# Kernel optimization log

Hardware: AMD Instinct MI355X
Metric: run time of the kernel (lower is better)

The kernel has to match this reference:

```python
import jax, jax.numpy as jnp
import numpy as np

B = 32
STRIDES = (8, 16, 32, 64, 128)
FEATS = ((192, 192), (96, 96), (48, 48), (24, 24), (12, 12))
IMG_H = IMG_W = 1536.0
OCTAVE_SCALE = 8.0
SCORE_THR = 0.05
IOU_THR = 0.6
MAX_NUM = 100
NMS_PRE = 1000
C = 2  # num foreground classes
RCLIP = float(np.log(1000.0 / 16.0))  # wh_ratio_clip from delta2bbox


def setup_inputs() -> dict:
    key = jax.random.key(0)
    ks = jax.random.split(key, 15)
    inp = {}
    i = 0
    for l, (h, w) in enumerate(FEATS):
        inp[f"cls{l}"] = jax.random.normal(ks[i], (B, C, h, w), jnp.float32); i += 1
        inp[f"bbox{l}"] = jax.random.normal(ks[i], (B, 4, h, w), jnp.float32) * 0.5; i += 1
        inp[f"ctr{l}"] = jax.random.normal(ks[i], (B, 1, h, w), jnp.float32); i += 1
    return inp


def _anchors(h, w, stride):
    # one square anchor of side OCTAVE_SCALE*stride per grid location
    xs = jnp.arange(w, dtype=jnp.float32) * stride
    ys = jnp.arange(h, dtype=jnp.float32) * stride
    cx = jnp.broadcast_to(xs[None, :], (h, w))
    cy = jnp.broadcast_to(ys[:, None], (h, w))
    half = 0.5 * OCTAVE_SCALE * stride
    return jnp.stack([cx - half, cy - half, cx + half, cy + half], -1).reshape(-1, 4)


def _decode(anchors, deltas):
    # standard delta2bbox (means=0, stds=1), clipped to image
    aw = anchors[..., 2] - anchors[..., 0]
    ah = anchors[..., 3] - anchors[..., 1]
    acx = anchors[..., 0] + 0.5 * aw
    acy = anchors[..., 1] + 0.5 * ah
    dx, dy = deltas[..., 0], deltas[..., 1]
    dw = jnp.clip(deltas[..., 2], -RCLIP, RCLIP)
    dh = jnp.clip(deltas[..., 3], -RCLIP, RCLIP)
    pcx = acx + dx * aw
    pcy = acy + dy * ah
    pw = aw * jnp.exp(dw)
    ph = ah * jnp.exp(dh)
    x1 = jnp.clip(pcx - 0.5 * pw, 0.0, IMG_W)
    y1 = jnp.clip(pcy - 0.5 * ph, 0.0, IMG_H)
    x2 = jnp.clip(pcx + 0.5 * pw, 0.0, IMG_W)
    y2 = jnp.clip(pcy + 0.5 * ph, 0.0, IMG_H)
    return jnp.stack([x1, y1, x2, y2], -1)


def _nms_single(boxes, boxes_off, scores, labels):
    # greedy class-aware NMS with fixed MAX_NUM output slots
    areas = (boxes_off[:, 2] - boxes_off[:, 0]) * (boxes_off[:, 3] - boxes_off[:, 1])

    def step(s, _):
        i = jnp.argmax(s)
        sc = s[i]
        valid = sc > 0.0
        b = boxes_off[i]
        ix1 = jnp.maximum(b[0], boxes_off[:, 0])
        iy1 = jnp.maximum(b[1], boxes_off[:, 1])
        ix2 = jnp.minimum(b[2], boxes_off[:, 2])
        iy2 = jnp.minimum(b[3], boxes_off[:, 3])
        inter = jnp.maximum(ix2 - ix1, 0.0) * jnp.maximum(iy2 - iy1, 0.0)
        iou = inter / jnp.maximum(areas[i] + areas - inter, 1e-6)
        s_new = jnp.where(valid & (iou > IOU_THR), -1.0, s)
        det = jnp.where(valid, jnp.concatenate([boxes[i], sc[None]]), jnp.zeros(5, jnp.float32))
        lab = jnp.where(valid, labels[i], -1)
        return s_new, (det, lab)

    _, (dets, labs) = jax.lax.scan(step, scores, None, length=MAX_NUM)
    return dets, labs


def _forward(cls0, cls1, cls2, cls3, cls4, bbox0, bbox1, bbox2, bbox3, bbox4,
             ctr0, ctr1, ctr2, ctr3, ctr4):
    clss = (cls0, cls1, cls2, cls3, cls4)
    bbs = (bbox0, bbox1, bbox2, bbox3, bbox4)
    ctrs = (ctr0, ctr1, ctr2, ctr3, ctr4)
    boxes_l, scores_l, ctr_l = [], [], []
    for (h, w), stride, cl, bb, ct in zip(FEATS, STRIDES, clss, bbs, ctrs):
        hw = h * w
        s = jax.nn.sigmoid(cl.reshape(B, C, hw).transpose(0, 2, 1))  # [B,HW,C]
        c = jax.nn.sigmoid(ct.reshape(B, hw))                        # [B,HW]
        d = bb.reshape(B, 4, hw).transpose(0, 2, 1)                  # [B,HW,4]
        anch = _anchors(h, w, stride)                                # [HW,4]
        k = min(NMS_PRE, hw)
        _, idx = jax.lax.top_k(s.max(-1) * c, k)                     # [B,k] nms_pre pre-selection
        s = jnp.take_along_axis(s, idx[..., None], 1)
        d = jnp.take_along_axis(d, idx[..., None], 1)
        c = jnp.take_along_axis(c, idx, 1)
        boxes_l.append(_decode(anch[idx], d))
        scores_l.append(s)
        ctr_l.append(c)
    boxes = jnp.concatenate(boxes_l, 1)    # [B,M,4]
    scores = jnp.concatenate(scores_l, 1)  # [B,M,C]
    ctr = jnp.concatenate(ctr_l, 1)        # [B,M]

    # multiclass_nms: scores * centerness factor, threshold, class-offset NMS
    cand_scores = (scores * ctr[..., None]).reshape(B, -1)              # [B,M*C]
    cand_scores = jnp.where(cand_scores > SCORE_THR, cand_scores, -1.0)
    cand_boxes = jnp.repeat(boxes, C, axis=1)                           # [B,M*C,4]
    labels = jnp.tile(jnp.arange(C, dtype=jnp.int32), boxes.shape[1])   # [M*C]
    offset = labels.astype(jnp.float32) * (IMG_W + 1.0)
    cand_off = cand_boxes + offset[None, :, None]
    dets, labs = jax.vmap(lambda b, bo, s: _nms_single(b, bo, s, labels))(
        cand_boxes, cand_off, cand_scores)
    return dets, labs  # [B,MAX_NUM,5] fp32, [B,MAX_NUM] int32 (-1 = empty slot)


def reference(cls0, cls1, cls2, cls3, cls4, bbox0, bbox1, bbox2, bbox3, bbox4,
              ctr0, ctr1, ctr2, ctr3, ctr4):
    return _forward(cls0, cls1, cls2, cls3, cls4, bbox0, bbox1, bbox2, bbox3, bbox4,
                    ctr0, ctr1, ctr2, ctr3, ctr4)
```

## Files before the change

### kernel.cpp

```cpp
#include <hip/hip_runtime.h>
#include <stdint.h>

#define BATCH 32
#define M_TOT 3720
#define NCAND 7440
#define NPAD 8192
#define SCORE_THR 0.05f
#define IOU_THR 0.6f
#define RCLIP 4.135166556742356f
#define IMG 1536.0f

__device__ __forceinline__ float sigf(float x) {
    return __fdiv_rn(1.0f, __fadd_rn(1.0f, expf(-x)));
}

struct P5 { const float* p[5]; };

template <int NPT>
__device__ __forceinline__ void select_level(
    const float* __restrict__ cls, const float* __restrict__ ctr,
    int b, int hw, int take, unsigned short* __restrict__ slots_out,
    unsigned long long* cu, unsigned* hist, unsigned* wtot,
    unsigned& sh_bin, unsigned& sh_krem, unsigned& sh_cnt)
{
    const int tid = threadIdx.x;
    float kv[NPT];
#pragma unroll
    for (int r = 0; r < NPT; ++r) {
        int i = tid + r * 1024;
        if (i < hw) {
            float s0 = sigf(cls[(size_t)(2*b)*hw + i]);
            float s1 = sigf(cls[(size_t)(2*b+1)*hw + i]);
            float sc = sigf(ctr[(size_t)b*hw + i]);
            kv[r] = __fmul_rn(fmaxf(s0, s1), sc);
        } else {
            kv[r] = -1.0f;
        }
    }

    int n;
    if (hw > 1000) {
        unsigned pref = 0, krem = 1000;
        for (int p = 0; p < 4; ++p) {
            const int shift = 24 - 8 * p;
            if (tid < 256) hist[tid] = 0;
            __syncthreads();
#pragma unroll
            for (int r = 0; r < NPT; ++r) {
                int i = tid + r * 1024;
                if (i < hw) {
                    unsigned u = __float_as_uint(kv[r]);
                    bool match = (p == 0) || ((u >> (shift + 8)) == pref);
                    if (match) atomicAdd(&hist[(u >> shift) & 255u], 1u);
                }
            }
            __syncthreads();
            unsigned h = 0, s = 0;
            if (tid < 256) {
                h = hist[tid];
                s = h;
#pragma unroll
                for (int d = 1; d < 64; d <<= 1) {
                    unsigned o = __shfl_down(s, d);
                    if ((tid & 63) + d < 64) s += o;
                }
                if ((tid & 63) == 0) wtot[tid >> 6] = s;
            }
            __syncthreads();
            if (tid < 256) {
                unsigned hi = 0;
                int wv = tid >> 6;
                for (int w2 = wv + 1; w2 < 4; ++w2) hi += wtot[w2];
                unsigned suf_incl = s + hi;
                unsigned suf_excl = suf_incl - h;
                if (suf_excl < krem && suf_incl >= krem) {
                    sh_bin = (unsigned)tid;
                    sh_krem = krem - suf_excl;
                    sh_cnt = 0;
                }
            }
            __syncthreads();
            pref = (pref << 8) | sh_bin;
            krem = sh_krem;
        }
        const unsigned T = pref;
#pragma unroll
        for (int r = 0; r < NPT; ++r) {
            int i = tid + r * 1024;
            if (i < hw) {
                unsigned u = __float_as_uint(kv[r]);
                if (u >= T) {
                    unsigned pos = atomicAdd(&sh_cnt, 1u);
                    if (pos < 2048u)
                        cu[pos] = (((unsigned long long)u) << 20) | (unsigned)(0xFFFFF - i);
                }
            }
        }
        __syncthreads();
        n = (int)sh_cnt; if (n > 2048) n = 2048;
    } else {
#pragma unroll
        for (int r = 0; r < NPT; ++r) {
            int i = tid + r * 1024;
            if (i < hw) {
                unsigned u = __float_as_uint(kv[r]);
                cu[i] = (((unsigned long long)u) << 20) | (unsigned)(0xFFFFF - i);
            }
        }
        n = hw;
        __syncthreads();
    }
    for (int a = tid; a < n; a += 1024) {
        unsigned long long ka = cu[a];
        int rank = 0;
        for (int q = 0; q < n; ++q) rank += (cu[q] > ka) ? 1 : 0;
        if (rank < take) {
            unsigned loc = 0xFFFFFu - (unsigned)(ka & 0xFFFFFu);
            slots_out[rank] = (unsigned short)loc;
        }
    }
}

__global__ __launch_bounds__(1024) void k_select(P5 CLS, P5 CT,
                                                 unsigned short* __restrict__ slots_g) {
    __shared__ unsigned long long cu[2048];
    __shared__ unsigned hist[256];
    __shared__ unsigned wtot[4];
    __shared__ unsigned sh_bin, sh_krem, sh_cnt;

    const int HWs[5]  = {36864, 9216, 2304, 576, 144};
    const int MOFF[5] = {0, 1000, 2000, 3000, 3576};

    const int blk = blockIdx.x;
    const int b = blk / 5, l = blk % 5;
    const int hw = HWs[l];
    const int take = (hw < 1000) ? hw : 1000;
    unsigned short* slots_out = slots_g + (size_t)b * M_TOT + MOFF[l];

    if (l == 0)      select_level<36>(CLS.p[0], CT.p[0], b, hw, take, slots_out, cu, hist, wtot, sh_bin, sh_krem, sh_cnt);
    else if (l == 1) select_level<9> (CLS.p[1], CT.p[1], b, hw, take, slots_out, cu, hist, wtot, sh_bin, sh_krem, sh_cnt);
    else if (l == 2) select_level<3> (CLS.p[2], CT.p[2], b, hw, take, slots_out, cu, hist, wtot, sh_bin, sh_krem, sh_cnt);
    else if (l == 3) select_level<1> (CLS.p[3], CT.p[3], b, hw, take, slots_out, cu, hist, wtot, sh_bin, sh_krem, sh_cnt);
    else             select_level<1> (CLS.p[4], CT.p[4], b, hw, take, slots_out, cu, hist, wtot, sh_bin, sh_krem, sh_cnt);
}

__global__ __launch_bounds__(256) void k_decode(P5 CLS, P5 BB, P5 CT,
                                                const unsigned short* __restrict__ slots_g,
                                                float* __restrict__ boxes_g,
                                                float* __restrict__ scores_g) {
    const int HWs[5]  = {36864, 9216, 2304, 576, 144};
    const int Ws[5]   = {192, 96, 48, 24, 12};
    const int STRs[5] = {8, 16, 32, 64, 128};
    int t = blockIdx.x * blockDim.x + threadIdx.x;
    if (t >= BATCH * M_TOT) return;
    int b = t / M_TOT;
    int m = t - b * M_TOT;
    int l;
    if (m < 1000)      l = 0;
    else if (m < 2000) l = 1;
    else if (m < 3000) l = 2;
    else if (m < 3576) l = 3;
    else               l = 4;
    const int hw = HWs[l], w = Ws[l], stride = STRs[l];
    int loc = slots_g[t];

    float ctv = sigf(CT.p[l][(size_t)b*hw + loc]);
    float sc0 = __fmul_rn(sigf(CLS.p[l][(size_t)(2*b+0)*hw + loc]), ctv);
    float sc1 = __fmul_rn(sigf(CLS.p[l][(size_t)(2*b+1)*hw + loc]), ctv);
    scores_g[(size_t)b * NCAND + 2*m + 0] = (sc0 > SCORE_THR) ? sc0 : -1.0f;
    scores_g[(size_t)b * NCAND + 2*m + 1] = (sc1 > SCORE_THR) ? sc1 : -1.0f;

    int yy = loc / w;
    int xx = loc - yy * w;
    const float* bb = BB.p[l];
    float d0 = bb[(size_t)(4*b+0)*hw + loc];
    float d1 = bb[(size_t)(4*b+1)*hw + loc];
    float d2 = bb[(size_t)(4*b+2)*hw + loc];
    float d3 = bb[(size_t)(4*b+3)*hw + loc];
    float a   = (float)(8 * stride);
    float acx = (float)(xx * stride);
    float acy = (float)(yy * stride);
    float dwv = fminf(fmaxf(d2, -RCLIP), RCLIP);
    float dhv = fminf(fmaxf(d3, -RCLIP), RCLIP);
    float pcx = __fadd_rn(acx, __fmul_rn(d0, a));
    float pcy = __fadd_rn(acy, __fmul_rn(d1, a));
    float pw  = __fmul_rn(a, expf(dwv));
    float ph  = __fmul_rn(a, expf(dhv));
    float* bx = boxes_g + (size_t)t * 4;
    bx[0] = fminf(fmaxf(__fsub_rn(pcx, __fmul_rn(0.5f, pw)), 0.0f), IMG);
    bx[1] = fminf(fmaxf(__fsub_rn(pcy, __fmul_rn(0.5f, ph)), 0.0f), IMG);
    bx[2] = fminf(fmaxf(__fadd_rn(pcx, __fmul_rn(0.5f, pw)), 0.0f), IMG);
    bx[3] = fminf(fmaxf(__fadd_rn(pcy, __fmul_rn(0.5f, ph)), 0.0f), IMG);
}

__global__ __launch_bounds__(1024) void k_nms(const float* __restrict__ boxes_g,
                                              const float* __restrict__ scores_g,
                                              float* __restrict__ out) {
    __shared__ unsigned long long cu[NPAD];
    const int b = blockIdx.x, tid = threadIdx.x;

    unsigned long long v[8];
    if (tid < 930) {
        const float4* s4 = (const float4*)(scores_g + (size_t)b * NCAND) + tid * 2;
        float4 a4 = s4[0], c4 = s4[1];
        float ss[8] = {a4.x, a4.y, a4.z, a4.w, c4.x, c4.y, c4.z, c4.w};
#pragma unroll
        for (int r = 0; r < 8; ++r) {
            int i = tid * 8 + r;
            v[r] = (ss[r] > 0.0f)
                ? ((((unsigned long long)(~__float_as_uint(ss[r]))) << 16) | (unsigned)i)
                : ~0ULL;
        }
    } else {
#pragma unroll
        for (int r = 0; r < 8; ++r) v[r] = ~0ULL;
    }

    for (unsigned kk = 2; kk <= NPAD; kk <<= 1) {
        for (unsigned j = kk >> 1; j > 0; j >>= 1) {
            if (j >= 512) {
                __syncthreads();
#pragma unroll
                for (int r = 0; r < 8; ++r) cu[tid * 8 + r] = v[r];
                __syncthreads();
#pragma unroll
                for (int r = 0; r < 8; ++r) {
                    unsigned i = tid * 8 + r;
                    unsigned long long pv = cu[i ^ j];
                    bool up = ((i & kk) == 0);
                    bool lower = ((i & j) == 0);
                    bool keepmin = (lower == up);
                    v[r] = keepmin ? (v[r] < pv ? v[r] : pv)
                                   : (v[r] > pv ? v[r] : pv);
                }
            } else if (j >= 8) {
                unsigned m = j >> 3;
#pragma unroll
                for (int r = 0; r < 8; ++r) {
                    unsigned long long pv = __shfl_xor(v[r], (int)m, 64);
                    unsigned i = tid * 8 + r;
                    bool up = ((i & kk) == 0);
                    bool lower = ((i & j) == 0);
                    bool keepmin = (lower == up);
                    v[r] = keepmin ? (v[r] < pv ? v[r] : pv)
                                   : (v[r] > pv ? v[r] : pv);
                }
            } else {
#pragma unroll
                for (int r = 0; r < 8; ++r) {
                    if ((r & j) == 0) {
                        unsigned i = tid * 8 + r;
                        bool up = ((i & kk) == 0);
                        unsigned long long a = v[r], b2 = v[r | j];
                        if ((a > b2) == up) { v[r] = b2; v[r | j] = a; }
                    }
                }
            }
        }
    }
    __syncthreads();
#pragma unroll
    for (int r = 0; r < 8; ++r) cu[tid * 8 + r] = v[r];
    __syncthreads();

    if (tid >= 64) return;

    const int lane = tid;
    const float4* bx4 = (const float4*)(boxes_g + (size_t)b * M_TOT * 4);
    float* keptL = (float*)(cu + NCAND);

    int kc = 0;
    bool done = false;

    for (int base = 0; base < NCAND && kc < 100 && !done; base += 64) {
        unsigned long long e = (base + lane < NCAND) ? cu[base + lane] : ~0ULL;
        bool valid = (e != ~0ULL);
        unsigned myidx = (unsigned)(e & 0xFFFFull);
        float myscore = __uint_as_float(~(unsigned)(e >> 16));
        int myc = (int)(myidx & 1u);
        float bx1 = 0, by1 = 0, bx2 = 0, by2 = 0;
        if (valid) {
            float4 vv = bx4[myidx >> 1];
            bx1 = vv.x; by1 = vv.y; bx2 = vv.z; by2 = vv.w;
        }
        float offv = myc ? (IMG + 1.0f) : 0.0f;
        float ox1 = __fadd_rn(bx1, offv), oy1 = __fadd_rn(by1, offv);
        float ox2 = __fadd_rn(bx2, offv), oy2 = __fadd_rn(by2, offv);
        float ca = __fmul_rn(__fsub_rn(ox2, ox1), __fsub_rn(oy2, oy1));
        float uni_s = fmaxf(__fsub_rn(__fadd_rn(ca, ca), ca), 1e-6f);
        bool mySticky = !(__fdiv_rn(ca, uni_s) > IOU_THR);

        const bool hasInvalid = (__ballot(!valid) != 0ULL);

        bool ov = false;
        if (valid) {
            for (int k = 0; k < kc && !ov; ++k) {
                float px1 = keptL[k*5+0], py1 = keptL[k*5+1];
                float px2 = keptL[k*5+2], py2 = keptL[k*5+3];
                float pa  = keptL[k*5+4];
                float ix1 = fmaxf(px1, ox1), iy1 = fmaxf(py1, oy1);
                float ix2 = fminf(px2, ox2), iy2 = fminf(py2, oy2);
                float inter = __fmul_rn(fmaxf(__fsub_rn(ix2, ix1), 0.0f),
                                        fmaxf(__fsub_rn(iy2, iy1), 0.0f));
                float uni = fmaxf(__fsub_rn(__fadd_rn(pa, ca), inter), 1e-6f);
                ov = (__fdiv_rn(inter, uni) > IOU_THR);
            }
        }
        bool myAlive = valid && !ov;
        unsigned long long aliveMask = __ballot(myAlive);

        while (aliveMask != 0ULL && kc < 100) {
            int j = __ffsll(aliveMask) - 1;
            float pbx1 = __shfl(bx1, j), pby1 = __shfl(by1, j);
            float pbx2 = __shfl(bx2, j), pby2 = __shfl(by2, j);
            float pox1 = __shfl(ox1, j), poy1 = __shfl(oy1, j);
            float pox2 = __shfl(ox2, j), poy2 = __shfl(oy2, j);
            float pca  = __shfl(ca, j);
            float psc  = __shfl(myscore, j);
            int   pc   = __shfl(myc, j);
            int   pst  = __shfl((int)mySticky, j);

            if (pst) {
                for (int t2 = kc + lane; t2 < 100; t2 += 64) {
                    float* dr = out + ((size_t)b * 100 + t2) * 5;
                    dr[0] = pbx1; dr[1] = pby1; dr[2] = pbx2; dr[3] = pby2; dr[4] = psc;
                    out[(size_t)BATCH * 500 + b * 100 + t2] = (float)pc;
                }
                kc = 100;
                done = true;
                break;
            }
            if (lane == 0) {
                float* dr = out + ((size_t)b * 100 + kc) * 5;
                dr[0] = pbx1; dr[1] = pby1; dr[2] = pbx2; dr[3] = pby2; dr[4] = psc;
                out[(size_t)BATCH * 500 + b * 100 + kc] = (float)pc;
                keptL[kc*5+0] = pox1; keptL[kc*5+1] = poy1;
                keptL[kc*5+2] = pox2; keptL[kc*5+3] = poy2;
                keptL[kc*5+4] = pca;
            }
            ++kc;
            if (myAlive && lane > j) {
                float ix1 = fmaxf(pox1, ox1), iy1 = fmaxf(poy1, oy1);
                float ix2 = fminf(pox2, ox2), iy2 = fminf(poy2, oy2);
                float inter = __fmul_rn(fmaxf(__fsub_rn(ix2, ix1), 0.0f),
                                        fmaxf(__fsub_rn(iy2, iy1), 0.0f));
                float uni = fmaxf(__fsub_rn(__fadd_rn(pca, ca), inter), 1e-6f);
                if (__fdiv_rn(inter, uni) > IOU_THR) myAlive = false;
            }
            if (lane == j) myAlive = false;
            aliveMask = __ballot(myAlive);
        }
        if (hasInvalid) break;
    }
    for (int t2 = kc + lane; t2 < 100; t2 += 64) {
        float* dr = out + ((size_t)b * 100 + t2) * 5;
        dr[0] = 0.0f; dr[1] = 0.0f; dr[2] = 0.0f; dr[3] = 0.0f; dr[4] = 0.0f;
        out[(size_t)BATCH * 500 + b * 100 + t2] = -1.0f;
    }
}

extern "C" void kernel_launch(void* const* d_in, const int* in_sizes, int n_in,
                              void* d_out, int out_size, void* d_ws, size_t ws_size,
                              hipStream_t stream) {
    static const int HW5[5] = {36864, 9216, 2304, 576, 144};
    int mc[5], mb[5], mt[5];
    bool found = false;
    for (int hyp = 0; hyp < 3 && !found; ++hyp) {
        bool ok = true;
        int tc[5], tb[5], tt[5];
        for (int l = 0; l < 5 && ok; ++l) {
            int ic, ib, it;
            if (hyp == 0)      { ic = 3*l;   ib = 3*l+1; it = 3*l+2; }
            else if (hyp == 1) { ic = l;     ib = 5+l;   it = 10+l;  }
            else               { ib = l;     ic = 5+l;   it = 10+l;  }
            if (in_sizes[ic] != 2*BATCH*HW5[l] ||
                in_sizes[ib] != 4*BATCH*HW5[l] ||
                in_sizes[it] != 1*BATCH*HW5[l]) ok = false;
            tc[l]=ic; tb[l]=ib; tt[l]=it;
        }
        if (ok) { for (int l=0;l<5;++l){mc[l]=tc[l];mb[l]=tb[l];mt[l]=tt[l];} found = true; }
    }
    if (!found) { for (int l=0;l<5;++l){mc[l]=3*l;mb[l]=3*l+1;mt[l]=3*l+2;} }

    P5 C, Bb, T;
    for (int l = 0; l < 5; ++l) {
        C.p[l]  = (const float*)d_in[mc[l]];
        Bb.p[l] = (const float*)d_in[mb[l]];
        T.p[l]  = (const float*)d_in[mt[l]];
    }

    uint8_t* w = (uint8_t*)d_ws;
    float*          boxes_g  = (float*)w;
    float*          scores_g = (float*)(w + 2097152);
    unsigned short* slots_g  = (unsigned short*)(w + 6291456);

    k_select<<<dim3(160),  dim3(1024), 0, stream>>>(C, T, slots_g);
    k_decode<<<dim3((BATCH*M_TOT + 255)/256), dim3(256), 0, stream>>>(
        C, Bb, T, slots_g, boxes_g, scores_g);
    k_nms   <<<dim3(BATCH), dim3(1024), 0, stream>>>(boxes_g, scores_g, (float*)d_out);
}
```

Before: 236.3 us.

## Fuse decode into NMS kernel, swizzle sort LDS, split kept lists per class

Folds the decode kernel into the NMS kernel, so each NMS thread decodes four candidates and builds its sort keys straight from registers. This drops one launch and the scores round trip through global memory. It also XOR-swizzles shared-memory indices in the bitonic sort to cut bank conflicts, and keeps separate kept-box lists per class so IoU checks only scan same-class boxes. The cost is that decode now runs on only 32 blocks instead of a wide grid, so there is less parallelism for the gathers.

```diff
diff --git a/kernel.cpp b/kernel.cpp
--- a/kernel.cpp
+++ b/kernel.cpp
@@ -13,6 +13,8 @@
 __device__ __forceinline__ float sigf(float x) {
     return __fdiv_rn(1.0f, __fadd_rn(1.0f, expf(-x)));
 }
+
+__device__ __forceinline__ unsigned swz(unsigned i) { return i ^ ((i >> 4) & 7u); }
 
 struct P5 { const float* p[5]; };
 
@@ -144,71 +146,66 @@
     else             select_level<1> (CLS.p[4], CT.p[4], b, hw, take, slots_out, cu, hist, wtot, sh_bin, sh_krem, sh_cnt);
 }
 
-__global__ __launch_bounds__(256) void k_decode(P5 CLS, P5 BB, P5 CT,
-                                                const unsigned short* __restrict__ slots_g,
-                                                float* __restrict__ boxes_g,
-                                                float* __restrict__ scores_g) {
+__global__ __launch_bounds__(1024) void k_nms(P5 CLS, P5 BB, P5 CT,
+                                              const unsigned short* __restrict__ slots_g,
+                                              float* __restrict__ boxes_g,
+                                              float* __restrict__ out) {
+    __shared__ unsigned long long cu[NPAD];
+    const int b = blockIdx.x, tid = threadIdx.x;
+
     const int HWs[5]  = {36864, 9216, 2304, 576, 144};
     const int Ws[5]   = {192, 96, 48, 24, 12};
     const int STRs[5] = {8, 16, 32, 64, 128};
-    int t = blockIdx.x * blockDim.x + threadIdx.x;
-    if (t >= BATCH * M_TOT) return;
-    int b = t / M_TOT;
-    int m = t - b * M_TOT;
-    int l;
-    if (m < 1000)      l = 0;
-    else if (m < 2000) l = 1;
-    else if (m < 3000) l = 2;
-    else if (m < 3576) l = 3;
-    else               l = 4;
-    const int hw = HWs[l], w = Ws[l], stride = STRs[l];
-    int loc = slots_g[t];
-
-    float ctv = sigf(CT.p[l][(size_t)b*hw + loc]);
-    float sc0 = __fmul_rn(sigf(CLS.p[l][(size_t)(2*b+0)*hw + loc]), ctv);
-    float sc1 = __fmul_rn(sigf(CLS.p[l][(size_t)(2*b+1)*hw + loc]), ctv);
-    scores_g[(size_t)b * NCAND + 2*m + 0] = (sc0 > SCORE_THR) ? sc0 : -1.0f;
-    scores_g[(size_t)b * NCAND + 2*m + 1] = (sc1 > SCORE_THR) ? sc1 : -1.0f;
-
-    int yy = loc / w;
-    int xx = loc - yy * w;
-    const float* bb = BB.p[l];
-    float d0 = bb[(size_t)(4*b+0)*hw + loc];
-    float d1 = bb[(size_t)(4*b+1)*hw + loc];
-    float d2 = bb[(size_t)(4*b+2)*hw + loc];
-    float d3 = bb[(size_t)(4*b+3)*hw + loc];
-    float a   = (float)(8 * stride);
-    float acx = (float)(xx * stride);
-    float acy = (float)(yy * stride);
-    float dwv = fminf(fmaxf(d2, -RCLIP), RCLIP);
-    float dhv = fminf(fmaxf(d3, -RCLIP), RCLIP);
-    float pcx = __fadd_rn(acx, __fmul_rn(d0, a));
-    float pcy = __fadd_rn(acy, __fmul_rn(d1, a));
-    float pw  = __fmul_rn(a, expf(dwv));
-    float ph  = __fmul_rn(a, expf(dhv));
-    float* bx = boxes_g + (size_t)t * 4;
-    bx[0] = fminf(fmaxf(__fsub_rn(pcx, __fmul_rn(0.5f, pw)), 0.0f), IMG);
-    bx[1] = fminf(fmaxf(__fsub_rn(pcy, __fmul_rn(0.5f, ph)), 0.0f), IMG);
-    bx[2] = fminf(fmaxf(__fadd_rn(pcx, __fmul_rn(0.5f, pw)), 0.0f), IMG);
-    bx[3] = fminf(fmaxf(__fadd_rn(pcy, __fmul_rn(0.5f, ph)), 0.0f), IMG);
-}
-
-__global__ __launch_bounds__(1024) void k_nms(const float* __restrict__ boxes_g,
-                                              const float* __restrict__ scores_g,
-                                              float* __restrict__ out) {
-    __shared__ unsigned long long cu[NPAD];
-    const int b = blockIdx.x, tid = threadIdx.x;
 
     unsigned long long v[8];
     if (tid < 930) {
-        const float4* s4 = (const float4*)(scores_g + (size_t)b * NCAND) + tid * 2;
-        float4 a4 = s4[0], c4 = s4[1];
-        float ss[8] = {a4.x, a4.y, a4.z, a4.w, c4.x, c4.y, c4.z, c4.w};
-#pragma unroll
-        for (int r = 0; r < 8; ++r) {
-            int i = tid * 8 + r;
-            v[r] = (ss[r] > 0.0f)
-                ? ((((unsigned long long)(~__float_as_uint(ss[r]))) << 16) | (unsigned)i)
+#pragma unroll
+        for (int q = 0; q < 4; ++q) {
+            int m = tid * 4 + q;
+            int l;
+            if (m < 1000)      l = 0;
+            else if (m < 2000) l = 1;
+            else if (m < 3000) l = 2;
+            else if (m < 3576) l = 3;
+            else               l = 4;
+            const int hw = HWs[l], w = Ws[l], stride = STRs[l];
+            int loc = slots_g[(size_t)b * M_TOT + m];
+
+            float ctv = sigf(CT.p[l][(size_t)b*hw + loc]);
+            float sc0 = __fmul_rn(sigf(CLS.p[l][(size_t)(2*b+0)*hw + loc]), ctv);
+            float sc1 = __fmul_rn(sigf(CLS.p[l][(size_t)(2*b+1)*hw + loc]), ctv);
+            sc0 = (sc0 > SCORE_THR) ? sc0 : -1.0f;
+            sc1 = (sc1 > SCORE_THR) ? sc1 : -1.0f;
+
+            int yy = loc / w;
+            int xx = loc - yy * w;
+            const float* bb = BB.p[l];
+            float d0 = bb[(size_t)(4*b+0)*hw + loc];
+            float d1 = bb[(size_t)(4*b+1)*hw + loc];
+            float d2 = bb[(size_t)(4*b+2)*hw + loc];
+            float d3 = bb[(size_t)(4*b+3)*hw + loc];
+            float a   = (float)(8 * stride);
+            float acx = (float)(xx * stride);
+            float acy = (float)(yy * stride);
+            float dwv = fminf(fmaxf(d2, -RCLIP), RCLIP);
+            float dhv = fminf(fmaxf(d3, -RCLIP), RCLIP);
+            float pcx = __fadd_rn(acx, __fmul_rn(d0, a));
+            float pcy = __fadd_rn(acy, __fmul_rn(d1, a));
+            float pw  = __fmul_rn(a, expf(dwv));
+            float ph  = __fmul_rn(a, expf(dhv));
+            float4 bx;
+            bx.x = fminf(fmaxf(__fsub_rn(pcx, __fmul_rn(0.5f, pw)), 0.0f), IMG);
+            bx.y = fminf(fmaxf(__fsub_rn(pcy, __fmul_rn(0.5f, ph)), 0.0f), IMG);
+            bx.z = fminf(fmaxf(__fadd_rn(pcx, __fmul_rn(0.5f, pw)), 0.0f), IMG);
+            bx.w = fminf(fmaxf(__fadd_rn(pcy, __fmul_rn(0.5f, ph)), 0.0f), IMG);
+            ((float4*)boxes_g)[(size_t)b * M_TOT + m] = bx;
+
+            int i0 = 2 * m;
+            v[2*q]   = (sc0 > 0.0f)
+                ? ((((unsigned long long)(~__float_as_uint(sc0))) << 16) | (unsigned)i0)
+                : ~0ULL;
+            v[2*q+1] = (sc1 > 0.0f)
+                ? ((((unsigned long long)(~__float_as_uint(sc1))) << 16) | (unsigned)(i0+1))
                 : ~0ULL;
         }
     } else {
@@ -221,12 +218,12 @@
             if (j >= 512) {
                 __syncthreads();
 #pragma unroll
-                for (int r = 0; r < 8; ++r) cu[tid * 8 + r] = v[r];
+                for (int r = 0; r < 8; ++r) cu[swz(tid * 8 + r)] = v[r];
                 __syncthreads();
 #pragma unroll
                 for (int r = 0; r < 8; ++r) {
                     unsigned i = tid * 8 + r;
-                    unsigned long long pv = cu[i ^ j];
+                    unsigned long long pv = cu[swz(i ^ j)];
                     bool up = ((i & kk) == 0);
                     bool lower = ((i & j) == 0);
                     bool keepmin = (lower == up);
@@ -260,20 +257,21 @@
     }
     __syncthreads();
 #pragma unroll
-    for (int r = 0; r < 8; ++r) cu[tid * 8 + r] = v[r];
+    for (int r = 0; r < 8; ++r) cu[swz(tid * 8 + r)] = v[r];
     __syncthreads();
 
     if (tid >= 64) return;
 
     const int lane = tid;
-    const float4* bx4 = (const float4*)(boxes_g + (size_t)b * M_TOT * 4);
-    float* keptL = (float*)(cu + NCAND);
-
-    int kc = 0;
+    const float4* bx4 = (const float4*)boxes_g + (size_t)b * M_TOT;
+    float* keptL0 = (float*)(cu + NCAND);
+    float* keptL1 = keptL0 + 500;
+
+    int kc = 0, kc0 = 0, kc1 = 0;
     bool done = false;
 
     for (int base = 0; base < NCAND && kc < 100 && !done; base += 64) {
-        unsigned long long e = (base + lane < NCAND) ? cu[base + lane] : ~0ULL;
+        unsigned long long e = (base + lane < NCAND) ? cu[swz(base + lane)] : ~0ULL;
         bool valid = (e != ~0ULL);
         unsigned myidx = (unsigned)(e & 0xFFFFull);
         float myscore = __uint_as_float(~(unsigned)(e >> 16));
@@ -294,10 +292,12 @@
 
         bool ov = false;
         if (valid) {
-            for (int k = 0; k < kc && !ov; ++k) {
-                float px1 = keptL[k*5+0], py1 = keptL[k*5+1];
-                float px2 = keptL[k*5+2], py2 = keptL[k*5+3];
-                float pa  = keptL[k*5+4];
+            const int kcc = myc ? kc1 : kc0;
+            const float* kl = myc ? keptL1 : keptL0;
+            for (int k = 0; k < kcc && !ov; ++k) {
+                float px1 = kl[k*5+0], py1 = kl[k*5+1];
+                float px2 = kl[k*5+2], py2 = kl[k*5+3];
+                float pa  = kl[k*5+4];
                 float ix1 = fmaxf(px1, ox1), iy1 = fmaxf(py1, oy1);
                 float ix2 = fminf(px2, ox2), iy2 = fminf(py2, oy2);
                 float inter = __fmul_rn(fmaxf(__fsub_rn(ix2, ix1), 0.0f),
@@ -334,12 +334,15 @@
                 float* dr = out + ((size_t)b * 100 + kc) * 5;
                 dr[0] = pbx1; dr[1] = pby1; dr[2] = pbx2; dr[3] = pby2; dr[4] = psc;
                 out[(size_t)BATCH * 500 + b * 100 + kc] = (float)pc;
-                keptL[kc*5+0] = pox1; keptL[kc*5+1] = poy1;
-                keptL[kc*5+2] = pox2; keptL[kc*5+3] = poy2;
-                keptL[kc*5+4] = pca;
+                float* kl = pc ? keptL1 : keptL0;
+                int  kcx = pc ? kc1 : kc0;
+                kl[kcx*5+0] = pox1; kl[kcx*5+1] = poy1;
+                kl[kcx*5+2] = pox2; kl[kcx*5+3] = poy2;
+                kl[kcx*5+4] = pca;
             }
             ++kc;
-            if (myAlive && lane > j) {
+            if (pc) ++kc1; else ++kc0;
+            if (myAlive && lane > j && myc == pc) {
                 float ix1 = fmaxf(pox1, ox1), iy1 = fmaxf(poy1, oy1);
                 float ix2 = fminf(pox2, ox2), iy2 = fminf(poy2, oy2);
                 float inter = __fmul_rn(fmaxf(__fsub_rn(ix2, ix1), 0.0f),
@@ -391,11 +394,9 @@
 
     uint8_t* w = (uint8_t*)d_ws;
     float*          boxes_g  = (float*)w;
-    float*          scores_g = (float*)(w + 2097152);
     unsigned short* slots_g  = (unsigned short*)(w + 6291456);
 
-    k_select<<<dim3(160),  dim3(1024), 0, stream>>>(C, T, slots_g);
-    k_decode<<<dim3((BATCH*M_TOT + 255)/256), dim3(256), 0, stream>>>(
-        C, Bb, T, slots_g, boxes_g, scores_g);
-    k_nms   <<<dim3(BATCH), dim3(1024), 0, stream>>>(boxes_g, scores_g, (float*)d_out);
+    k_select<<<dim3(160), dim3(1024), 0, stream>>>(C, T, slots_g);
+    k_nms   <<<dim3(BATCH), dim3(1024), 0, stream>>>(C, Bb, T, slots_g, boxes_g,
+                                                     (float*)d_out);
 }
```

Result: no change. 237.5 us (+0.5%).

## Replace quadratic rank selection with bitonic sort, swizzle LDS, split NMS per class

Applied to the files above, without the earlier changes.

In k_select, the O(n^2) rank counting over up to 2048 candidates is replaced by a 2048-element bitonic sort held in registers, using wavefront shuffles for short strides and LDS for long strides. Shared-memory indices in both bitonic sorts are XOR-swizzled to reduce bank conflicts. In k_nms, kept boxes are stored in separate per-class lists, so each candidate is only tested against kept boxes of its own class and cross-class IoU checks are skipped. That last change relies on the class offset making cross-class overlap impossible. The sort pays extra sync rounds in exchange for removing the quadratic scan.

```diff
diff --git a/kernel.cpp b/kernel.cpp
--- a/kernel.cpp
+++ b/kernel.cpp
@@ -13,6 +13,8 @@
 __device__ __forceinline__ float sigf(float x) {
     return __fdiv_rn(1.0f, __fadd_rn(1.0f, expf(-x)));
 }
+
+__device__ __forceinline__ unsigned swz(unsigned i) { return i ^ ((i >> 4) & 7u); }
 
 struct P5 { const float* p[5]; };
 
@@ -38,7 +40,7 @@
         }
     }
 
-    int n;
+    unsigned long long v[2];
     if (hw > 1000) {
         unsigned pref = 0, krem = 1000;
         for (int p = 0; p < 4; ++p) {
@@ -84,6 +86,8 @@
             krem = sh_krem;
         }
         const unsigned T = pref;
+        cu[tid] = ~0ULL; cu[tid + 1024] = ~0ULL;
+        __syncthreads();
 #pragma unroll
         for (int r = 0; r < NPT; ++r) {
             int i = tid + r * 1024;
@@ -92,30 +96,73 @@
                 if (u >= T) {
                     unsigned pos = atomicAdd(&sh_cnt, 1u);
                     if (pos < 2048u)
-                        cu[pos] = (((unsigned long long)u) << 20) | (unsigned)(0xFFFFF - i);
+                        cu[pos] = ~((((unsigned long long)u) << 20) | (unsigned)(0xFFFFF - i));
                 }
             }
         }
         __syncthreads();
-        n = (int)sh_cnt; if (n > 2048) n = 2048;
+        v[0] = cu[tid * 2 + 0];
+        v[1] = cu[tid * 2 + 1];
     } else {
 #pragma unroll
-        for (int r = 0; r < NPT; ++r) {
-            int i = tid + r * 1024;
+        for (int r = 0; r < 2; ++r) {
+            int i = tid * 2 + r;
             if (i < hw) {
-                unsigned u = __float_as_uint(kv[r]);
-                cu[i] = (((unsigned long long)u) << 20) | (unsigned)(0xFFFFF - i);
-            }
-        }
-        n = hw;
-        __syncthreads();
-    }
-    for (int a = tid; a < n; a += 1024) {
-        unsigned long long ka = cu[a];
-        int rank = 0;
-        for (int q = 0; q < n; ++q) rank += (cu[q] > ka) ? 1 : 0;
+                float s0 = sigf(cls[(size_t)(2*b)*hw + i]);
+                float s1 = sigf(cls[(size_t)(2*b+1)*hw + i]);
+                float sc = sigf(ctr[(size_t)b*hw + i]);
+                unsigned u = __float_as_uint(__fmul_rn(fmaxf(s0, s1), sc));
+                v[r] = ~((((unsigned long long)u) << 20) | (unsigned)(0xFFFFF - i));
+            } else {
+                v[r] = ~0ULL;
+            }
+        }
+    }
+
+    for (unsigned kk = 2; kk <= 2048; kk <<= 1) {
+        for (unsigned j = kk >> 1; j > 0; j >>= 1) {
+            if (j >= 128) {
+                __syncthreads();
+                cu[swz(tid * 2 + 0)] = v[0];
+                cu[swz(tid * 2 + 1)] = v[1];
+                __syncthreads();
+#pragma unroll
+                for (int r = 0; r < 2; ++r) {
+                    unsigned i = tid * 2 + r;
+                    unsigned long long pv = cu[swz(i ^ j)];
+                    bool up = ((i & kk) == 0);
+                    bool lower = ((i & j) == 0);
+                    bool keepmin = (lower == up);
+                    v[r] = keepmin ? (v[r] < pv ? v[r] : pv)
+                                   : (v[r] > pv ? v[r] : pv);
+                }
+            } else if (j >= 2) {
+                unsigned m = j >> 1;
+#pragma unroll
+                for (int r = 0; r < 2; ++r) {
+                    unsigned long long pv = __shfl_xor(v[r], (int)m, 64);
+                    unsigned i = tid * 2 + r;
+                    bool up = ((i & kk) == 0);
+                    bool lower = ((i & j) == 0);
+                    bool keepmin = (lower == up);
+                    v[r] = keepmin ? (v[r] < pv ? v[r] : pv)
+                                   : (v[r] > pv ? v[r] : pv);
+                }
+            } else {
+                unsigned i = tid * 2;
+                bool up = ((i & kk) == 0);
+                if ((v[0] > v[1]) == up) {
+                    unsigned long long t = v[0]; v[0] = v[1]; v[1] = t;
+                }
+            }
+        }
+    }
+#pragma unroll
+    for (int r = 0; r < 2; ++r) {
+        int rank = tid * 2 + r;
         if (rank < take) {
-            unsigned loc = 0xFFFFFu - (unsigned)(ka & 0xFFFFFu);
+            unsigned long long c = ~v[r];
+            unsigned loc = 0xFFFFFu - (unsigned)(c & 0xFFFFFu);
             slots_out[rank] = (unsigned short)loc;
         }
     }
@@ -221,12 +268,12 @@
             if (j >= 512) {
                 __syncthreads();
 #pragma unroll
-                for (int r = 0; r < 8; ++r) cu[tid * 8 + r] = v[r];
+                for (int r = 0; r < 8; ++r) cu[swz(tid * 8 + r)] = v[r];
                 __syncthreads();
 #pragma unroll
                 for (int r = 0; r < 8; ++r) {
                     unsigned i = tid * 8 + r;
-                    unsigned long long pv = cu[i ^ j];
+                    unsigned long long pv = cu[swz(i ^ j)];
                     bool up = ((i & kk) == 0);
                     bool lower = ((i & j) == 0);
                     bool keepmin = (lower == up);
@@ -260,20 +307,21 @@
     }
     __syncthreads();
 #pragma unroll
-    for (int r = 0; r < 8; ++r) cu[tid * 8 + r] = v[r];
+    for (int r = 0; r < 8; ++r) cu[swz(tid * 8 + r)] = v[r];
     __syncthreads();
 
     if (tid >= 64) return;
 
     const int lane = tid;
-    const float4* bx4 = (const float4*)(boxes_g + (size_t)b * M_TOT * 4);
-    float* keptL = (float*)(cu + NCAND);
-
-    int kc = 0;
+    const float4* bx4 = (const float4*)boxes_g + (size_t)b * M_TOT;
+    float* keptL0 = (float*)(cu + NCAND);
+    float* keptL1 = keptL0 + 500;
+
+    int kc = 0, kc0 = 0, kc1 = 0;
     bool done = false;
 
     for (int base = 0; base < NCAND && kc < 100 && !done; base += 64) {
-        unsigned long long e = (base + lane < NCAND) ? cu[base + lane] : ~0ULL;
+        unsigned long long e = (base + lane < NCAND) ? cu[swz(base + lane)] : ~0ULL;
         bool valid = (e != ~0ULL);
         unsigned myidx = (unsigned)(e & 0xFFFFull);
         float myscore = __uint_as_float(~(unsigned)(e >> 16));
@@ -294,10 +342,12 @@
 
         bool ov = false;
         if (valid) {
-            for (int k = 0; k < kc && !ov; ++k) {
-                float px1 = keptL[k*5+0], py1 = keptL[k*5+1];
-                float px2 = keptL[k*5+2], py2 = keptL[k*5+3];
-                float pa  = keptL[k*5+4];
+            const int kcc = myc ? kc1 : kc0;
+            const float* kl = myc ? keptL1 : keptL0;
+            for (int k = 0; k < kcc && !ov; ++k) {
+                float px1 = kl[k*5+0], py1 = kl[k*5+1];
+                float px2 = kl[k*5+2], py2 = kl[k*5+3];
+                float pa  = kl[k*5+4];
                 float ix1 = fmaxf(px1, ox1), iy1 = fmaxf(py1, oy1);
                 float ix2 = fminf(px2, ox2), iy2 = fminf(py2, oy2);
                 float inter = __fmul_rn(fmaxf(__fsub_rn(ix2, ix1), 0.0f),
@@ -334,12 +384,15 @@
                 float* dr = out + ((size_t)b * 100 + kc) * 5;
                 dr[0] = pbx1; dr[1] = pby1; dr[2] = pbx2; dr[3] = pby2; dr[4] = psc;
                 out[(size_t)BATCH * 500 + b * 100 + kc] = (float)pc;
-                keptL[kc*5+0] = pox1; keptL[kc*5+1] = poy1;
-                keptL[kc*5+2] = pox2; keptL[kc*5+3] = poy2;
-                keptL[kc*5+4] = pca;
+                float* kl = pc ? keptL1 : keptL0;
+                int  kcx = pc ? kc1 : kc0;
+                kl[kcx*5+0] = pox1; kl[kcx*5+1] = poy1;
+                kl[kcx*5+2] = pox2; kl[kcx*5+3] = poy2;
+                kl[kcx*5+4] = pca;
             }
             ++kc;
-            if (myAlive && lane > j) {
+            if (pc) ++kc1; else ++kc0;
+            if (myAlive && lane > j && myc == pc) {
                 float ix1 = fmaxf(pox1, ox1), iy1 = fmaxf(poy1, oy1);
                 float ix2 = fminf(pox2, ox2), iy2 = fminf(poy2, oy2);
                 float inter = __fmul_rn(fmaxf(__fsub_rn(ix2, ix1), 0.0f),
@@ -394,7 +447,7 @@
     float*          scores_g = (float*)(w + 2097152);
     unsigned short* slots_g  = (unsigned short*)(w + 6291456);
 
-    k_select<<<dim3(160),  dim3(1024), 0, stream>>>(C, T, slots_g);
+    k_select<<<dim3(160), dim3(1024), 0, stream>>>(C, T, slots_g);
     k_decode<<<dim3((BATCH*M_TOT + 255)/256), dim3(256), 0, stream>>>(
         C, Bb, T, slots_g, boxes_g, scores_g);
     k_nms   <<<dim3(BATCH), dim3(1024), 0, stream>>>(boxes_g, scores_g, (float*)d_out);
```

New measurement: 225.6 us. 1.05x faster.
